# Performance work log

Hardware: AMD Instinct MI355X
Metric: run time of the kernel (lower is better)

## Reference

```python
import jax, jax.numpy as jnp
import numpy as np

ALPHA = 20.0 / 100.0  # dt / tau


def setup_inputs() -> dict:
    key = jax.random.key(0)
    k1, k2, k3, k4 = jax.random.split(key, 4)
    B, T, I, H = 128, 4096, 128, 512
    inputs = jax.random.normal(k1, (B, T, I), dtype=jnp.float32)
    hidden = jnp.zeros((B, H), dtype=jnp.float32)
    w_in = jax.random.normal(k2, (H, I), dtype=jnp.float32) / np.sqrt(I)
    w_rec = jax.random.normal(k3, (H, H), dtype=jnp.float32) / np.sqrt(H)
    b_rec = jnp.zeros((H,), dtype=jnp.float32)
    w_out = jax.random.normal(k4, (1, H), dtype=jnp.float32) * (2.0 / np.sqrt(H))
    b_out = jnp.zeros((1,), dtype=jnp.float32)
    return {"inputs": inputs, "hidden": hidden, "w_in": w_in, "w_rec": w_rec,
            "b_rec": b_rec, "w_out": w_out, "b_out": b_out}


def reference(inputs, hidden, w_in, w_rec, b_rec, w_out, b_out):
    # inputs: (B, T, I); hidden: (B, H)
    # Precompute input projection for all timesteps (batched GEMM).
    inp_proj = jnp.einsum('bti,hi->tbh', inputs, w_in)  # (T, B, H)

    def step(h, x_t):
        rec = jnp.einsum('bh,gh->bg', h, w_rec) + b_rec  # w_rec @ h per Linear
        activated = jax.nn.relu(x_t + rec)
        h_new = (1.0 - ALPHA) * h + ALPHA * activated
        return h_new, h_new

    h_final, states = jax.lax.scan(step, hidden, inp_proj)  # states: (T, B, H)
    # Linear readout at every timestep: y(t) = w_out h(t) + b_out, squeezed.
    outputs = jnp.einsum('tbh,oh->bto', states, w_out)[..., 0] + b_out[0]  # (B, T)
    return outputs, h_final
```

## Files before the change

kernel.cpp:

```cpp
#include <hip/hip_runtime.h>
#include <hip/hip_bf16.h>

#define B_ 128
#define T_ 4096
#define I_ 128
#define H_ 512

typedef __attribute__((ext_vector_type(8))) short short8;
typedef __attribute__((ext_vector_type(4))) float f32x4;
typedef __attribute__((ext_vector_type(4))) unsigned short us4;

__device__ __forceinline__ unsigned short f2bf(float f) {
  union { float f; unsigned int u; } v; v.f = f;
  unsigned int r = v.u + 0x7FFFu + ((v.u >> 16) & 1u);
  return (unsigned short)(r >> 16);
}

__device__ __forceinline__ short8 cvt8(f32x4 a, f32x4 b) {
  union { short8 s; unsigned short u[8]; } r;
#pragma unroll
  for (int j = 0; j < 4; ++j) { r.u[j] = f2bf(a[j]); r.u[4 + j] = f2bf(b[j]); }
  return r.s;
}

__device__ __forceinline__ short8 ld_h16(const unsigned short* p) {
  union { short8 s; unsigned long long u[2]; } r;
  r.u[0] = __hip_atomic_load((const unsigned long long*)p,
                             __ATOMIC_RELAXED, __HIP_MEMORY_SCOPE_AGENT);
  r.u[1] = __hip_atomic_load((const unsigned long long*)(p + 4),
                             __ATOMIC_RELAXED, __HIP_MEMORY_SCOPE_AGENT);
  return r.s;
}
__device__ __forceinline__ void st_h8(unsigned short* p, us4 v) {
  union { us4 v; unsigned long long u; } r; r.v = v;
  __hip_atomic_store((unsigned long long*)p, r.u,
                     __ATOMIC_RELAXED, __HIP_MEMORY_SCOPE_AGENT);
}

#define WBF_BYTES  ((size_t)(H_ * H_ + H_ * I_) * 2)
#define CNT_OFF    WBF_BYTES
#define CNT_STRIDE 1024
#define CNT_BYTES  ((size_t)8 * CNT_STRIDE)
#define HX_OFF     (CNT_OFF + CNT_BYTES)
#define HX_BYTES   ((size_t)8 * 2 * 16 * H_ * 2)
#define YP_OFF     (((HX_OFF + HX_BYTES) + 63) & ~(size_t)63)
#define YP_BYTES   ((size_t)8 * T_ * 8 * 16 * 4)
#define WS_NEED    (YP_OFF + YP_BYTES)

__global__ void cvt_w_kernel(const float* __restrict__ w_rec,
                             const float* __restrict__ w_in,
                             unsigned short* __restrict__ wbf,
                             unsigned int* __restrict__ cnt) {
  int i = blockIdx.x * blockDim.x + threadIdx.x;
  if (i < H_ * H_) wbf[i] = f2bf(w_rec[i]);
  if (i < H_ * I_) wbf[H_ * H_ + i] = f2bf(w_in[i]);
  if (cnt != nullptr && i < 8)
    __hip_atomic_store(&cnt[(size_t)i * (CNT_STRIDE / 4)], 0u,
                       __ATOMIC_RELAXED, __HIP_MEMORY_SCOPE_AGENT);
}

__global__ __launch_bounds__(256, 1)
void rnn_pair_kernel(const float* __restrict__ inputs,
                     const float* __restrict__ hidden,
                     const float* __restrict__ b_rec,
                     const float* __restrict__ w_out,
                     const unsigned short* __restrict__ wbf,
                     unsigned short* __restrict__ hx,
                     unsigned int* __restrict__ cnt,
                     float* __restrict__ ypartial,
                     float* __restrict__ hfin) {
  const int tid  = threadIdx.x;
  const int wave = tid >> 6;
  const int lane = tid & 63;
  const int q    = lane >> 4;
  const int c    = lane & 15;
  const int pair = blockIdx.x & 7;
  const int half = blockIdx.x >> 3;
  const int wip  = half * 4 + wave;
  const int r0   = pair * 16;
  const int n0   = half * 256 + wave * 64;

  short8 wr[16][4], wi[4][4];
  {
    const unsigned short* wrp = wbf + (size_t)(n0 + c) * H_ + q * 8;
    const unsigned short* wip_ = wbf + (size_t)H_ * H_ + (size_t)(n0 + c) * I_ + q * 8;
#pragma unroll
    for (int kk = 0; kk < 16; ++kk)
#pragma unroll
      for (int nt = 0; nt < 4; ++nt)
        wr[kk][nt] = *(const short8*)(wrp + (size_t)nt * 16 * H_ + kk * 32);
#pragma unroll
    for (int kk = 0; kk < 4; ++kk)
#pragma unroll
      for (int nt = 0; nt < 4; ++nt)
        wi[kk][nt] = *(const short8*)(wip_ + (size_t)nt * 16 * I_ + kk * 32);
  }

  f32x4 hreg[4], brec[4], wout[4];
#pragma unroll
  for (int nt = 0; nt < 4; ++nt)
#pragma unroll
    for (int r = 0; r < 4; ++r) {
      const int g = n0 + nt * 16 + q * 4 + r;
      hreg[nt][r] = hidden[(size_t)(r0 + c) * H_ + g];
      brec[nt][r] = b_rec[g];
      wout[nt][r] = w_out[g];
    }

  unsigned int* mycnt = (unsigned int*)((char*)cnt + (size_t)pair * CNT_STRIDE);
  unsigned short* hx0 = hx + (size_t)(pair * 2) * 16 * H_;
  unsigned short* hx1 = hx0 + 16 * H_;

  const float* xbase = inputs + (size_t)(r0 + c) * T_ * I_ + q * 8;

  f32x4 xn[4][2];
#pragma unroll
  for (int kk = 0; kk < 4; ++kk) {
    xn[kk][0] = *(const f32x4*)(xbase + kk * 32);
    xn[kk][1] = *(const f32x4*)(xbase + kk * 32 + 4);
  }

#pragma unroll
  for (int nt = 0; nt < 4; ++nt) {
    us4 hb;
#pragma unroll
    for (int r = 0; r < 4; ++r) hb[r] = f2bf(hreg[nt][r]);
    st_h8(hx0 + (size_t)c * H_ + n0 + nt * 16 + q * 4, hb);
  }
  asm volatile("s_waitcnt vmcnt(0)" ::: "memory");
  if (lane == 0)
    __hip_atomic_fetch_add(mycnt, 1u, __ATOMIC_RELAXED, __HIP_MEMORY_SCOPE_AGENT);

  for (int t = 0; t < T_; ++t) {
    short8 xc[4];
#pragma unroll
    for (int kk = 0; kk < 4; ++kk) xc[kk] = cvt8(xn[kk][0], xn[kk][1]);
    f32x4 acc[4];
#pragma unroll
    for (int nt = 0; nt < 4; ++nt) acc[nt] = (f32x4){0.f, 0.f, 0.f, 0.f};
#pragma unroll
    for (int kk = 0; kk < 4; ++kk)
#pragma unroll
      for (int nt = 0; nt < 4; ++nt)
        acc[nt] = __builtin_amdgcn_mfma_f32_16x16x32_bf16(wi[kk][nt], xc[kk], acc[nt], 0, 0, 0);

    __builtin_amdgcn_sched_barrier(0);

    const unsigned target = 8u * (unsigned)(t + 1);
    while (__hip_atomic_load(mycnt, __ATOMIC_RELAXED, __HIP_MEMORY_SCOPE_AGENT) < target) {}
    asm volatile("" ::: "memory");

    const unsigned short* hr = ((t & 1) ? hx1 : hx0) + (size_t)c * H_ + q * 8;

    short8 hb8[8];
#pragma unroll
    for (int kk = 0; kk < 8; ++kk) hb8[kk] = ld_h16(hr + kk * 32);
#pragma unroll
    for (int kk = 0; kk < 16; ++kk) {
      short8 b = hb8[kk & 7];
      if (kk < 8) hb8[kk & 7] = ld_h16(hr + (kk + 8) * 32);
#pragma unroll
      for (int nt = 0; nt < 4; ++nt)
        acc[nt] = __builtin_amdgcn_mfma_f32_16x16x32_bf16(wr[kk][nt], b, acc[nt], 0, 0, 0);
    }

    const bool pub = (t + 1 < T_);
    unsigned short* hw = (t & 1) ? hx0 : hx1;
    float yl = 0.f;
#pragma unroll
    for (int nt = 0; nt < 4; ++nt) {
      us4 hb;
#pragma unroll
      for (int r = 0; r < 4; ++r) {
        float act = fmaxf(acc[nt][r] + brec[nt][r], 0.f);
        float h = hreg[nt][r] * 0.8f + 0.2f * act;
        hreg[nt][r] = h;
        hb[r] = f2bf(h);
        yl = __builtin_fmaf(wout[nt][r], h, yl);
      }
      if (pub) st_h8(hw + (size_t)c * H_ + n0 + nt * 16 + q * 4, hb);
    }

    __builtin_amdgcn_sched_barrier(0);
    {
      const float* xp = xbase + (size_t)((t + 1 < T_) ? (t + 1) : t) * I_;
#pragma unroll
      for (int kk = 0; kk < 4; ++kk) {
        xn[kk][0] = *(const f32x4*)(xp + kk * 32);
        xn[kk][1] = *(const f32x4*)(xp + kk * 32 + 4);
      }
    }
    __builtin_amdgcn_sched_barrier(0);
    if (pub) {
      asm volatile("s_waitcnt vmcnt(8)" ::: "memory");
      if (lane == 0)
        __hip_atomic_fetch_add(mycnt, 1u, __ATOMIC_RELAXED, __HIP_MEMORY_SCOPE_AGENT);
    }

    yl += __shfl_xor(yl, 16, 64);
    yl += __shfl_xor(yl, 32, 64);
    if (q == 0)
      ypartial[(((size_t)pair * T_ + t) * 8 + wip) * 16 + c] = yl;
  }

#pragma unroll
  for (int nt = 0; nt < 4; ++nt)
    *(f32x4*)(hfin + (size_t)(r0 + c) * H_ + n0 + nt * 16 + q * 4) = hreg[nt];
}

__global__ void reduce_y_kernel(const float* __restrict__ ypartial,
                                const float* __restrict__ b_out,
                                float* __restrict__ out) {
  const int idx = blockIdx.x * 256 + threadIdx.x;
  const int t = idx & (T_ - 1);
  const int r = idx >> 12;
  const int p = r >> 4, b = r & 15;
  const float* yp = ypartial + (((size_t)p * T_ + t) * 8) * 16 + b;
  float s = b_out[0];
#pragma unroll
  for (int w = 0; w < 8; ++w) s += yp[w * 16];
  out[(size_t)r * T_ + t] = s;
}

template <bool WBF16>
__global__ __launch_bounds__(512, 2)
void rnn_kernel_fb(const float* __restrict__ inputs,
                   const float* __restrict__ hidden,
                   const float* __restrict__ w_in_f,
                   const float* __restrict__ w_rec_f,
                   const float* __restrict__ b_rec,
                   const float* __restrict__ w_out,
                   const float* __restrict__ b_out,
                   const unsigned short* __restrict__ wbf,
                   float* __restrict__ out) {
  __shared__ alignas(16) unsigned short hs[2][16][520];
  __shared__ alignas(16) float ypart[2][8][16];

  const int tid  = threadIdx.x;
  const int wave = tid >> 6;
  const int lane = tid & 63;
  const int q    = lane >> 4;
  const int c    = lane & 15;
  const int r0   = blockIdx.x * 16;
  const int n0   = wave * 64;

  for (int e = tid; e < 16 * H_; e += 512) {
    int rr = e >> 9, cc = e & (H_ - 1);
    hs[0][rr][cc] = f2bf(hidden[(size_t)(r0 + rr) * H_ + cc]);
  }

  f32x4 hreg[4];
  float brec[4], wout[4];
#pragma unroll
  for (int nt = 0; nt < 4; ++nt) {
    const int col = n0 + nt * 16 + c;
    brec[nt] = b_rec[col];
    wout[nt] = w_out[col];
#pragma unroll
    for (int r = 0; r < 4; ++r)
      hreg[nt][r] = hidden[(size_t)(r0 + q * 4 + r) * H_ + col];
  }
  const float bout = b_out[0];
  __syncthreads();

  const unsigned short* wrecb = wbf;
  const unsigned short* winb  = wbf + H_ * H_;
  const size_t wr_off = (size_t)(n0 + c) * H_ + q * 8;
  const size_t wi_off = (size_t)(n0 + c) * I_ + q * 8;
  const float* xbase = inputs + (size_t)(r0 + c) * T_ * I_ + q * 8;

#pragma unroll 2
  for (int t = 0; t < T_; ++t) {
    const int rb = t & 1, wb = rb ^ 1;
    f32x4 xf[4][2];
    const float* xp = xbase + (size_t)t * I_;
#pragma unroll
    for (int kk = 0; kk < 4; ++kk) {
      xf[kk][0] = *(const f32x4*)(xp + kk * 32);
      xf[kk][1] = *(const f32x4*)(xp + kk * 32 + 4);
    }
    f32x4 acc[4];
#pragma unroll
    for (int nt = 0; nt < 4; ++nt) acc[nt] = (f32x4){0.f, 0.f, 0.f, 0.f};
    const unsigned short* hrow = &hs[rb][c][q * 8];
#pragma unroll
    for (int kk = 0; kk < 16; ++kk) {
      short8 a = *(const short8*)(hrow + kk * 32);
#pragma unroll
      for (int nt = 0; nt < 4; ++nt) {
        short8 b;
        if constexpr (WBF16) {
          b = *(const short8*)(wrecb + wr_off + (size_t)nt * 16 * H_ + kk * 32);
        } else {
          const float* p = w_rec_f + wr_off + (size_t)nt * 16 * H_ + kk * 32;
          b = cvt8(*(const f32x4*)p, *(const f32x4*)(p + 4));
        }
        acc[nt] = __builtin_amdgcn_mfma_f32_16x16x32_bf16(a, b, acc[nt], 0, 0, 0);
      }
    }
#pragma unroll
    for (int kk = 0; kk < 4; ++kk) {
      short8 ax = cvt8(xf[kk][0], xf[kk][1]);
#pragma unroll
      for (int nt = 0; nt < 4; ++nt) {
        short8 b;
        if constexpr (WBF16) {
          b = *(const short8*)(winb + wi_off + (size_t)nt * 16 * I_ + kk * 32);
        } else {
          const float* p = w_in_f + wi_off + (size_t)nt * 16 * I_ + kk * 32;
          b = cvt8(*(const f32x4*)p, *(const f32x4*)(p + 4));
        }
        acc[nt] = __builtin_amdgcn_mfma_f32_16x16x32_bf16(ax, b, acc[nt], 0, 0, 0);
      }
    }
    float yp2[4] = {0.f, 0.f, 0.f, 0.f};
#pragma unroll
    for (int nt = 0; nt < 4; ++nt) {
#pragma unroll
      for (int r = 0; r < 4; ++r) {
        float act = fmaxf(acc[nt][r] + brec[nt], 0.f);
        float h = hreg[nt][r] * 0.8f + 0.2f * act;
        hreg[nt][r] = h;
        hs[wb][q * 4 + r][n0 + nt * 16 + c] = f2bf(h);
        yp2[r] = __builtin_fmaf(wout[nt], h, yp2[r]);
      }
    }
#pragma unroll
    for (int off = 8; off >= 1; off >>= 1) {
#pragma unroll
      for (int r = 0; r < 4; ++r) yp2[r] += __shfl_xor(yp2[r], off, 64);
    }
    if (c == 0)
      *(f32x4*)&ypart[wb][wave][q * 4] = (f32x4){yp2[0], yp2[1], yp2[2], yp2[3]};
    __syncthreads();
    if (tid < 16) {
      float s = bout;
#pragma unroll
      for (int w = 0; w < 8; ++w) s += ypart[wb][w][tid];
      out[(size_t)(r0 + tid) * T_ + t] = s;
    }
  }
  float* hfin = out + (size_t)B_ * T_;
#pragma unroll
  for (int nt = 0; nt < 4; ++nt)
#pragma unroll
    for (int r = 0; r < 4; ++r)
      hfin[(size_t)(r0 + q * 4 + r) * H_ + n0 + nt * 16 + c] = hreg[nt][r];
}

extern "C" void kernel_launch(void* const* d_in, const int* in_sizes, int n_in,
                              void* d_out, int out_size, void* d_ws, size_t ws_size,
                              hipStream_t stream) {
  const float* inputs = (const float*)d_in[0];
  const float* hidden = (const float*)d_in[1];
  const float* w_in   = (const float*)d_in[2];
  const float* w_rec  = (const float*)d_in[3];
  const float* b_rec  = (const float*)d_in[4];
  const float* w_out  = (const float*)d_in[5];
  const float* b_out  = (const float*)d_in[6];
  float* out = (float*)d_out;

  if (ws_size >= WS_NEED) {
    unsigned short* wbf = (unsigned short*)d_ws;
    unsigned int*   cnt = (unsigned int*)((char*)d_ws + CNT_OFF);
    unsigned short* hx  = (unsigned short*)((char*)d_ws + HX_OFF);
    float*          yp  = (float*)((char*)d_ws + YP_OFF);
    float*          hfin = out + (size_t)B_ * T_;
    cvt_w_kernel<<<dim3((H_ * H_ + 255) / 256), dim3(256), 0, stream>>>(w_rec, w_in, wbf, cnt);
    rnn_pair_kernel<<<dim3(16), dim3(256), 0, stream>>>(
        inputs, hidden, b_rec, w_out, wbf, hx, cnt, yp, hfin);
    reduce_y_kernel<<<dim3((B_ * T_) / 256), dim3(256), 0, stream>>>(yp, b_out, out);
  } else if (ws_size >= WBF_BYTES) {
    unsigned short* wbf = (unsigned short*)d_ws;
    cvt_w_kernel<<<dim3((H_ * H_ + 255) / 256), dim3(256), 0, stream>>>(w_rec, w_in, wbf, nullptr);
    rnn_kernel_fb<true><<<dim3(8), dim3(512), 0, stream>>>(
        inputs, hidden, w_in, w_rec, b_rec, w_out, b_out, wbf, out);
  } else {
    rnn_kernel_fb<false><<<dim3(8), dim3(512), 0, stream>>>(
        inputs, hidden, w_in, w_rec, b_rec, w_out, b_out, (const unsigned short*)nullptr, out);
  }
}
```

Measured before the change: 27.74 ms.

## Interleave four batch groups per block to hide inter-block sync latency

Each block now processes four 16-row batch groups in round-robin instead of one, so the grid shrinks from 16 to 4 blocks. The spin-wait for the partner block's hidden state for one group overlaps with compute on the other groups, and the publish counter increment is deferred by one group so store latency is hidden. w_in fragments move from registers to LDS to free registers for the quadrupled hidden state. The trade-off is roughly four times more serial work per block on a 256-CU device, which cuts parallelism sharply.

```diff
diff --git a/kernel.cpp b/kernel.cpp
--- a/kernel.cpp
+++ b/kernel.cpp
@@ -60,7 +60,7 @@
 }
 
 __global__ __launch_bounds__(256, 1)
-void rnn_pair_kernel(const float* __restrict__ inputs,
+void rnn_quad_kernel(const float* __restrict__ inputs,
                      const float* __restrict__ hidden,
                      const float* __restrict__ b_rec,
                      const float* __restrict__ w_out,
@@ -74,138 +74,182 @@
   const int lane = tid & 63;
   const int q    = lane >> 4;
   const int c    = lane & 15;
-  const int pair = blockIdx.x & 7;
-  const int half = blockIdx.x >> 3;
+  const int half = blockIdx.x & 1;
+  const int pg   = blockIdx.x >> 1;
   const int wip  = half * 4 + wave;
-  const int r0   = pair * 16;
   const int n0   = half * 256 + wave * 64;
 
-  short8 wr[16][4], wi[4][4];
+  __shared__ short8 wiL[4][16][64];
+
+  short8 wr[16][4];
   {
     const unsigned short* wrp = wbf + (size_t)(n0 + c) * H_ + q * 8;
-    const unsigned short* wip_ = wbf + (size_t)H_ * H_ + (size_t)(n0 + c) * I_ + q * 8;
 #pragma unroll
     for (int kk = 0; kk < 16; ++kk)
 #pragma unroll
       for (int nt = 0; nt < 4; ++nt)
         wr[kk][nt] = *(const short8*)(wrp + (size_t)nt * 16 * H_ + kk * 32);
+  }
+  {
+    const unsigned short* wip_ = wbf + (size_t)H_ * H_ + (size_t)(n0 + c) * I_ + q * 8;
 #pragma unroll
     for (int kk = 0; kk < 4; ++kk)
 #pragma unroll
       for (int nt = 0; nt < 4; ++nt)
-        wi[kk][nt] = *(const short8*)(wip_ + (size_t)nt * 16 * I_ + kk * 32);
-  }
-
-  f32x4 hreg[4], brec[4], wout[4];
+        wiL[wave][kk * 4 + nt][lane] = *(const short8*)(wip_ + (size_t)nt * 16 * I_ + kk * 32);
+  }
+  __syncthreads();
+
+  f32x4 brec[4], wout[4];
 #pragma unroll
   for (int nt = 0; nt < 4; ++nt)
 #pragma unroll
     for (int r = 0; r < 4; ++r) {
       const int g = n0 + nt * 16 + q * 4 + r;
-      hreg[nt][r] = hidden[(size_t)(r0 + c) * H_ + g];
       brec[nt][r] = b_rec[g];
       wout[nt][r] = w_out[g];
     }
 
-  unsigned int* mycnt = (unsigned int*)((char*)cnt + (size_t)pair * CNT_STRIDE);
-  unsigned short* hx0 = hx + (size_t)(pair * 2) * 16 * H_;
-  unsigned short* hx1 = hx0 + 16 * H_;
-
-  const float* xbase = inputs + (size_t)(r0 + c) * T_ * I_ + q * 8;
-
-  f32x4 xn[4][2];
-#pragma unroll
-  for (int kk = 0; kk < 4; ++kk) {
-    xn[kk][0] = *(const f32x4*)(xbase + kk * 32);
-    xn[kk][1] = *(const f32x4*)(xbase + kk * 32 + 4);
-  }
-
-#pragma unroll
-  for (int nt = 0; nt < 4; ++nt) {
-    us4 hb;
-#pragma unroll
-    for (int r = 0; r < 4; ++r) hb[r] = f2bf(hreg[nt][r]);
-    st_h8(hx0 + (size_t)c * H_ + n0 + nt * 16 + q * 4, hb);
-  }
-  asm volatile("s_waitcnt vmcnt(0)" ::: "memory");
-  if (lane == 0)
-    __hip_atomic_fetch_add(mycnt, 1u, __ATOMIC_RELAXED, __HIP_MEMORY_SCOPE_AGENT);
-
-  for (int t = 0; t < T_; ++t) {
-    short8 xc[4];
-#pragma unroll
-    for (int kk = 0; kk < 4; ++kk) xc[kk] = cvt8(xn[kk][0], xn[kk][1]);
-    f32x4 acc[4];
-#pragma unroll
-    for (int nt = 0; nt < 4; ++nt) acc[nt] = (f32x4){0.f, 0.f, 0.f, 0.f};
-#pragma unroll
-    for (int kk = 0; kk < 4; ++kk)
-#pragma unroll
-      for (int nt = 0; nt < 4; ++nt)
-        acc[nt] = __builtin_amdgcn_mfma_f32_16x16x32_bf16(wi[kk][nt], xc[kk], acc[nt], 0, 0, 0);
-
-    __builtin_amdgcn_sched_barrier(0);
-
-    const unsigned target = 8u * (unsigned)(t + 1);
-    while (__hip_atomic_load(mycnt, __ATOMIC_RELAXED, __HIP_MEMORY_SCOPE_AGENT) < target) {}
-    asm volatile("" ::: "memory");
-
-    const unsigned short* hr = ((t & 1) ? hx1 : hx0) + (size_t)c * H_ + q * 8;
-
-    short8 hb8[8];
-#pragma unroll
-    for (int kk = 0; kk < 8; ++kk) hb8[kk] = ld_h16(hr + kk * 32);
-#pragma unroll
-    for (int kk = 0; kk < 16; ++kk) {
-      short8 b = hb8[kk & 7];
-      if (kk < 8) hb8[kk & 7] = ld_h16(hr + (kk + 8) * 32);
-#pragma unroll
-      for (int nt = 0; nt < 4; ++nt)
-        acc[nt] = __builtin_amdgcn_mfma_f32_16x16x32_bf16(wr[kk][nt], b, acc[nt], 0, 0, 0);
-    }
-
-    const bool pub = (t + 1 < T_);
-    unsigned short* hw = (t & 1) ? hx0 : hx1;
-    float yl = 0.f;
+  f32x4 hreg[4][4];
+  const float* xb[4];
+  unsigned int* cnts[4];
+  unsigned short* hx0s[4];
+  unsigned short* hx1s[4];
+#pragma unroll
+  for (int s = 0; s < 4; ++s) {
+    const int pair = pg * 4 + s;
+    const int r0 = pair * 16;
+    xb[s]   = inputs + (size_t)(r0 + c) * T_ * I_ + q * 8;
+    cnts[s] = (unsigned int*)((char*)cnt + (size_t)pair * CNT_STRIDE);
+    hx0s[s] = hx + (size_t)(pair * 2) * 16 * H_;
+    hx1s[s] = hx0s[s] + 16 * H_;
+#pragma unroll
+    for (int nt = 0; nt < 4; ++nt)
+      hreg[s][nt] = *(const f32x4*)&hidden[(size_t)(r0 + c) * H_ + n0 + nt * 16 + q * 4];
+  }
+
+#pragma unroll
+  for (int s = 0; s < 4; ++s)
 #pragma unroll
     for (int nt = 0; nt < 4; ++nt) {
       us4 hb;
 #pragma unroll
-      for (int r = 0; r < 4; ++r) {
-        float act = fmaxf(acc[nt][r] + brec[nt][r], 0.f);
-        float h = hreg[nt][r] * 0.8f + 0.2f * act;
-        hreg[nt][r] = h;
-        hb[r] = f2bf(h);
-        yl = __builtin_fmaf(wout[nt][r], h, yl);
-      }
-      if (pub) st_h8(hw + (size_t)c * H_ + n0 + nt * 16 + q * 4, hb);
-    }
-
-    __builtin_amdgcn_sched_barrier(0);
-    {
-      const float* xp = xbase + (size_t)((t + 1 < T_) ? (t + 1) : t) * I_;
-#pragma unroll
-      for (int kk = 0; kk < 4; ++kk) {
-        xn[kk][0] = *(const f32x4*)(xp + kk * 32);
-        xn[kk][1] = *(const f32x4*)(xp + kk * 32 + 4);
-      }
-    }
-    __builtin_amdgcn_sched_barrier(0);
-    if (pub) {
-      asm volatile("s_waitcnt vmcnt(8)" ::: "memory");
-      if (lane == 0)
-        __hip_atomic_fetch_add(mycnt, 1u, __ATOMIC_RELAXED, __HIP_MEMORY_SCOPE_AGENT);
-    }
-
-    yl += __shfl_xor(yl, 16, 64);
-    yl += __shfl_xor(yl, 32, 64);
-    if (q == 0)
-      ypartial[(((size_t)pair * T_ + t) * 8 + wip) * 16 + c] = yl;
-  }
-
-#pragma unroll
-  for (int nt = 0; nt < 4; ++nt)
-    *(f32x4*)(hfin + (size_t)(r0 + c) * H_ + n0 + nt * 16 + q * 4) = hreg[nt];
+      for (int r = 0; r < 4; ++r) hb[r] = f2bf(hreg[s][nt][r]);
+      st_h8(hx0s[s] + (size_t)c * H_ + n0 + nt * 16 + q * 4, hb);
+    }
+  asm volatile("s_waitcnt vmcnt(0)" ::: "memory");
+  if (lane == 0) {
+#pragma unroll
+    for (int s = 0; s < 4; ++s)
+      __hip_atomic_fetch_add(cnts[s], 1u, __ATOMIC_RELAXED, __HIP_MEMORY_SCOPE_AGENT);
+  }
+
+  f32x4 xn[4][2];
+  short8 xc[4];
+  {
+    const float* xp = xb[0];
+#pragma unroll
+    for (int kk = 0; kk < 4; ++kk) {
+      xn[kk][0] = *(const f32x4*)(xp + kk * 32);
+      xn[kk][1] = *(const f32x4*)(xp + kk * 32 + 4);
+    }
+#pragma unroll
+    for (int kk = 0; kk < 4; ++kk) xc[kk] = cvt8(xn[kk][0], xn[kk][1]);
+  }
+
+  unsigned int* pend = nullptr;
+
+  for (int t = 0; t < T_; ++t) {
+#pragma unroll
+    for (int s = 0; s < 4; ++s) {
+      {
+        const int tn = (s == 3) ? ((t + 1 < T_) ? t + 1 : t) : t;
+        const float* xp = xb[(s + 1) & 3] + (size_t)tn * I_;
+#pragma unroll
+        for (int kk = 0; kk < 4; ++kk) {
+          xn[kk][0] = *(const f32x4*)(xp + kk * 32);
+          xn[kk][1] = *(const f32x4*)(xp + kk * 32 + 4);
+        }
+      }
+
+      f32x4 acc[4];
+#pragma unroll
+      for (int nt = 0; nt < 4; ++nt) acc[nt] = (f32x4){0.f, 0.f, 0.f, 0.f};
+#pragma unroll
+      for (int kk = 0; kk < 4; ++kk)
+#pragma unroll
+        for (int nt = 0; nt < 4; ++nt) {
+          short8 wfrag = wiL[wave][kk * 4 + nt][lane];
+          acc[nt] = __builtin_amdgcn_mfma_f32_16x16x32_bf16(wfrag, xc[kk], acc[nt], 0, 0, 0);
+        }
+      __builtin_amdgcn_sched_barrier(0);
+
+      {
+        const unsigned target = 8u * (unsigned)(t + 1);
+        while (__hip_atomic_load(cnts[s], __ATOMIC_RELAXED, __HIP_MEMORY_SCOPE_AGENT) < target) {}
+        asm volatile("" ::: "memory");
+      }
+
+      const unsigned short* hr = ((t & 1) ? hx1s[s] : hx0s[s]) + (size_t)c * H_ + q * 8;
+      short8 hb4[4];
+#pragma unroll
+      for (int kk = 0; kk < 4; ++kk) hb4[kk] = ld_h16(hr + kk * 32);
+#pragma unroll
+      for (int kk = 0; kk < 16; ++kk) {
+        short8 b = hb4[kk & 3];
+        if (kk < 12) hb4[kk & 3] = ld_h16(hr + (kk + 4) * 32);
+#pragma unroll
+        for (int nt = 0; nt < 4; ++nt)
+          acc[nt] = __builtin_amdgcn_mfma_f32_16x16x32_bf16(wr[kk][nt], b, acc[nt], 0, 0, 0);
+      }
+
+      float yl = 0.f;
+      us4 hbv[4];
+#pragma unroll
+      for (int nt = 0; nt < 4; ++nt) {
+#pragma unroll
+        for (int r = 0; r < 4; ++r) {
+          float act = fmaxf(acc[nt][r] + brec[nt][r], 0.f);
+          float h = hreg[s][nt][r] * 0.8f + 0.2f * act;
+          hreg[s][nt][r] = h;
+          hbv[nt][r] = f2bf(h);
+          yl = __builtin_fmaf(wout[nt][r], h, yl);
+        }
+      }
+
+      if (pend != nullptr) {
+        asm volatile("s_waitcnt vmcnt(0)" ::: "memory");
+        if (lane == 0)
+          __hip_atomic_fetch_add(pend, 1u, __ATOMIC_RELAXED, __HIP_MEMORY_SCOPE_AGENT);
+      }
+
+      if (t + 1 < T_) {
+        unsigned short* hw = (t & 1) ? hx0s[s] : hx1s[s];
+#pragma unroll
+        for (int nt = 0; nt < 4; ++nt)
+          st_h8(hw + (size_t)c * H_ + n0 + nt * 16 + q * 4, hbv[nt]);
+        pend = cnts[s];
+      } else {
+        pend = nullptr;
+      }
+
+      yl += __shfl_xor(yl, 16, 64);
+      yl += __shfl_xor(yl, 32, 64);
+      if (q == 0)
+        ypartial[(((size_t)(pg * 4 + s) * T_ + t) * 8 + wip) * 16 + c] = yl;
+
+#pragma unroll
+      for (int kk = 0; kk < 4; ++kk) xc[kk] = cvt8(xn[kk][0], xn[kk][1]);
+    }
+  }
+
+#pragma unroll
+  for (int s = 0; s < 4; ++s) {
+    const int r0 = (pg * 4 + s) * 16;
+#pragma unroll
+    for (int nt = 0; nt < 4; ++nt)
+      *(f32x4*)(hfin + (size_t)(r0 + c) * H_ + n0 + nt * 16 + q * 4) = hreg[s][nt];
+  }
 }
 
 __global__ void reduce_y_kernel(const float* __restrict__ ypartial,
@@ -367,7 +411,7 @@
     float*          yp  = (float*)((char*)d_ws + YP_OFF);
     float*          hfin = out + (size_t)B_ * T_;
     cvt_w_kernel<<<dim3((H_ * H_ + 255) / 256), dim3(256), 0, stream>>>(w_rec, w_in, wbf, cnt);
-    rnn_pair_kernel<<<dim3(16), dim3(256), 0, stream>>>(
+    rnn_quad_kernel<<<dim3(4), dim3(256), 0, stream>>>(
         inputs, hidden, b_rec, w_out, wbf, hx, cnt, yp, hfin);
     reduce_y_kernel<<<dim3((B_ * T_) / 256), dim3(256), 0, stream>>>(yp, b_out, out);
   } else if (ws_size >= WBF_BYTES) {
```

Measured after the change: 106.4 ms. 284% more time.
